# Kernel tuning notes

Hardware: AMD Instinct MI355X
Metric: run time of the kernel (lower is better)

Reference implementation:

```python
import jax, jax.numpy as jnp
import numpy as np

V, D, B, P = 50000, 128, 1024, 50
N, E = B * P, B * P
SCALE = 12.0


def _norm(x):
    return jnp.linalg.norm(x, axis=-1, keepdims=True)


def setup_inputs():
    key = jax.random.key(0)
    ks = jax.random.split(key, 32)
    stdv = 1.0 / np.sqrt(D)

    def u(k, shape):
        return jax.random.uniform(k, shape, minval=-stdv, maxval=stdv, dtype=jnp.float32)

    iid = jax.random.randint(ks[0], (N,), 0, V)
    # edges stay inside each session's node block [g*P, (g+1)*P)
    base = jnp.repeat(jnp.arange(B) * P, P)
    edge_src = base + jax.random.randint(ks[1], (E,), 0, P)
    edge_dst = base + jax.random.randint(ks[2], (E,), 0, P)
    node_gid = jnp.repeat(jnp.arange(B), P)          # session id per node
    last_nodes = jnp.arange(B) * P + (P - 1)          # nodes with data['last']==1
    edge_w = jax.random.uniform(ks[3], (E,), minval=0.1, maxval=1.0)
    edge_t = jax.random.uniform(ks[4], (E,))
    params = dict(
        embedding=u(ks[5], (V, D)),
        W1=u(ks[6], (D, 2 * D)), W2=u(ks[7], (D, 2 * D)),
        gru_wih=u(ks[8], (3 * D, 4 * D)), gru_whh=u(ks[9], (3 * D, D)),
        gru_bih=u(ks[10], (3 * D,)), gru_bhh=u(ks[11], (3 * D,)),
        Wxr=u(ks[12], (D, D)), bxr=u(ks[13], (D,)),
        Wxz=u(ks[14], (D, D)), bxz=u(ks[15], (D,)),
        Wxh=u(ks[16], (D, D)), bxh=u(ks[17], (D,)),
        Whr=u(ks[18], (D, D)), bhr=u(ks[19], (D,)),
        Whz=u(ks[20], (D, D)), bhz=u(ks[21], (D,)),
        Whh=u(ks[22], (D, D)), bhh=u(ks[23], (D,)),
        fc_u=u(ks[24], (D, D)),
        fc_vw=u(ks[25], (D, D)), fc_vb=u(ks[26], (D,)),
        fc_e=u(ks[27], (D,)),
        fc_sr=u(ks[28], (2 * D, D)),
    )
    return dict(iid=iid, edge_src=edge_src, edge_dst=edge_dst, node_gid=node_gid,
                last_nodes=last_nodes, edge_w=edge_w, edge_t=edge_t, **params)


def reference(iid, edge_src, edge_dst, node_gid, last_nodes, edge_w, edge_t,
              embedding, W1, W2, gru_wih, gru_whh, gru_bih, gru_bhh,
              Wxr, bxr, Wxz, bxz, Wxh, bxh, Whr, bhr, Whz, bhz, Whh, bhh,
              fc_u, fc_vw, fc_vb, fc_e, fc_sr):
    segN = lambda d, ids: jax.ops.segment_sum(d, ids, num_segments=N)
    feat = embedding[iid]
    feat = feat / (_norm(feat) + 1e-12)

    # --- GGNNLayer (num_layers=1): weighted-mean over in-edges and reversed graph ---
    ws_in = segN(edge_w, edge_dst)
    ws_out = segN(edge_w, edge_src)
    m_in = segN(feat[edge_src] * edge_w[:, None], edge_dst)
    m_out = segN(feat[edge_dst] * edge_w[:, None], edge_src)
    neigh1 = m_in / jnp.where(ws_in > 0, ws_in, 1.0)[:, None]   # zero-degree -> 0 (DGL default)
    neigh2 = m_out / jnp.where(ws_out > 0, ws_out, 1.0)[:, None]
    hn = jnp.concatenate([neigh1 @ W1, neigh2 @ W2], axis=1)    # [N, 4D]
    gi = hn @ gru_wih.T + gru_bih
    gh = feat @ gru_whh.T + gru_bhh
    ir, iz, inn = jnp.split(gi, 3, axis=1)
    hr, hz, hnn = jnp.split(gh, 3, axis=1)
    r = jax.nn.sigmoid(ir + hr)
    z = jax.nn.sigmoid(iz + hz)
    n = jnp.tanh(inn + r * hnn)
    feat = (1.0 - z) * n + z * feat                              # GRUCell update
    feat = feat / jnp.maximum(_norm(feat), 1e-12)                # F.normalize

    # --- GraphGRUODE: one RK4 step on [0, t_end]; per-eval time-filtered symmetric GCN ---
    x = feat
    no_self = edge_src != edge_dst

    def gcn(h, em, W, b):
        # DGL GraphConv norm='both' on the masked graph + its reverse edges
        deg = segN(em, edge_src) + segN(em, edge_dst)
        nrm = jnp.maximum(deg, 1.0) ** -0.5
        hs = h * nrm[:, None]
        me = em[:, None]
        agg = segN(hs[edge_src] * me, edge_dst) + segN(hs[edge_dst] * me, edge_src)
        return (agg * nrm[:, None]) @ W + b

    def f(tv, h):
        em = ((edge_t <= tv) & no_self).astype(h.dtype)
        xr = gcn(x, em, Wxr, bxr)
        xz = gcn(x, em, Wxz, bxz)
        xh = gcn(x, em, Wxh, bxh)
        r_ = jax.nn.sigmoid(xr + gcn(h, em, Whr, bhr))
        z_ = jax.nn.sigmoid(xz + gcn(h, em, Whz, bhz))
        u_ = jnp.tanh(xh + gcn(r_ * h, em, Whh, bhh))
        dh = (1.0 - z_) * (u_ - h)
        return dh / jnp.maximum(_norm(dh), 1e-12)                # F.normalize

    dt = edge_t.max()
    k1 = f(jnp.float32(0.0), feat)
    k2 = f(dt * 0.5, feat + dt * 0.5 * k1)
    k3 = f(dt * 0.5, feat + dt * 0.5 * k2)
    k4 = f(dt, feat + dt * k3)
    feat = feat + (dt / 6.0) * (k1 + 2.0 * k2 + 2.0 * k3 + k4)
    feat = feat / _norm(feat)                                    # torch code divides with no eps here

    # --- AttnReadout (batch_norm disabled, fc_out is None) ---
    fu = feat @ fc_u
    fv = feat[last_nodes] @ fc_vw + fc_vb                        # [B, D]
    e = jax.nn.sigmoid(fu + fv[node_gid]) @ fc_e                 # [N]
    emax = jax.ops.segment_max(e, node_gid, num_segments=B)
    ee = jnp.exp(e - emax[node_gid])
    alpha = ee / jax.ops.segment_sum(ee, node_gid, num_segments=B)[node_gid]
    sr_g = jax.ops.segment_sum(feat * alpha[:, None], node_gid, num_segments=B)
    sr = jnp.concatenate([feat[last_nodes], sr_g], axis=1) @ fc_sr
    sr = sr / (_norm(sr) + 1e-12)

    target = embedding / (_norm(embedding) + 1e-12)
    logits = sr @ target.T                                       # [B, V]
    return jax.nn.log_softmax(SCALE * logits, axis=-1)
```

## Files before the change

kernel.cpp:

```cpp
#include <hip/hip_runtime.h>
#include <math.h>

constexpr int V_ = 50000, D_ = 128, B_ = 1024, P_ = 50;
constexpr int N_ = 51200, E_ = 51200;
constexpr long long NS_ = (long long)N_ * D_;
constexpr float SCALE_ = 12.0f;
constexpr int NBN_L = (V_ + 127) / 128;
constexpr int NBN_P = 392;

typedef unsigned short u16;
typedef __attribute__((ext_vector_type(8))) unsigned short u16x8;
typedef __attribute__((ext_vector_type(8))) __bf16 bf16x8;
typedef __attribute__((ext_vector_type(4))) float f32x4;

static __device__ __forceinline__ float wsum(float v) {
    #pragma unroll
    for (int o = 32; o; o >>= 1) v += __shfl_xor(v, o, 64);
    return v;
}
static __device__ __forceinline__ float wmax(float v) {
    #pragma unroll
    for (int o = 32; o; o >>= 1) v = fmaxf(v, __shfl_xor(v, o, 64));
    return v;
}
static __device__ __forceinline__ float fsig(float x) { return 1.f / (1.f + __expf(-x)); }
static __device__ __forceinline__ float ftanh(float x) { return 2.f / (1.f + __expf(-2.f * x)) - 1.f; }
static __device__ __forceinline__ u16 f2b(float x) {
    unsigned u = __float_as_uint(x);
    u += 0x7fffu + ((u >> 16) & 1u);
    return (u16)(u >> 16);
}
static __device__ __forceinline__ float b2f(u16 u) {
    return __uint_as_float(((unsigned)u) << 16);
}
static __device__ __forceinline__ float redlr(float v) {
    v += __shfl_xor(v, 1, 64); v += __shfl_xor(v, 2, 64);
    v += __shfl_xor(v, 4, 64); v += __shfl_xor(v, 8, 64);
    return v;
}

__global__ void k_embcv(const float* __restrict__ emb, u16* __restrict__ embb,
                        float* __restrict__ rnv) {
    int row = blockIdx.x * 4 + (threadIdx.x >> 6);
    if (row >= V_) return;
    int l = threadIdx.x & 63;
    const float* p = emb + (long long)row * D_;
    float a = p[l], b = p[l + 64];
    float ss = wsum(a * a + b * b);
    if (l == 0) rnv[row] = 1.f / (sqrtf(ss) + 1e-12f);
    u16* q = embb + (long long)row * D_;
    q[l] = f2b(a); q[l + 64] = f2b(b);
}

__global__ void k_dtmax(const float* __restrict__ et, float* __restrict__ dt) {
    __shared__ float s[1024];
    float m = 0.f;
    for (int i = threadIdx.x; i < E_; i += 1024) m = fmaxf(m, et[i]);
    s[threadIdx.x] = m; __syncthreads();
    for (int o = 512; o; o >>= 1) {
        if (threadIdx.x < o) s[threadIdx.x] = fmaxf(s[threadIdx.x], s[threadIdx.x + o]);
        __syncthreads();
    }
    if (threadIdx.x == 0) *dt = s[0];
}

__global__ void k_feat0(const u16* __restrict__ embb, const float* __restrict__ rnv,
                        const int* __restrict__ iid, u16* __restrict__ featb) {
    int row = blockIdx.x * 4 + (threadIdx.x >> 6);
    int l = threadIdx.x & 63;
    int id = iid[row];
    const u16* p = embb + (long long)id * D_;
    float s = rnv[id];
    u16* qb = featb + (long long)row * D_;
    qb[l] = f2b(b2f(p[l]) * s); qb[l + 64] = f2b(b2f(p[l + 64]) * s);
}

__global__ void k_aggA_g(const int* __restrict__ esrc, const int* __restrict__ edst,
                         const float* __restrict__ ew, const u16* __restrict__ featb,
                         u16* __restrict__ m_in, u16* __restrict__ m_out) {
    __shared__ float sfeat[P_ * D_];
    __shared__ float smin[P_ * D_];
    __shared__ float smout[P_ * D_];
    __shared__ int ses[P_], sed[P_];
    __shared__ float sw[P_], swin[P_], swout[P_];
    int g = blockIdx.x, t = threadIdx.x;
    int n0 = g * P_;
    long long base = (long long)n0 * D_;
    for (int i = t; i < P_ * D_; i += 256) {
        sfeat[i] = b2f(featb[base + i]);
        smin[i] = 0.f; smout[i] = 0.f;
    }
    if (t < P_) {
        int E0 = g * P_ + t;
        ses[t] = esrc[E0] - n0;
        sed[t] = edst[E0] - n0;
        sw[t] = ew[E0];
    }
    __syncthreads();
    int d = t & 127;
    for (int e = 0; e < P_; e++) {
        int ls = ses[e], ld = sed[e];
        float w = sw[e];
        if (t < 128) smin[ld * D_ + d] += sfeat[ls * D_ + d] * w;
        else         smout[ls * D_ + d] += sfeat[ld * D_ + d] * w;
    }
    if (t < P_) {
        float wi = 0.f, wo = 0.f;
        for (int e = 0; e < P_; e++) {
            if (sed[e] == t) wi += sw[e];
            if (ses[e] == t) wo += sw[e];
        }
        swin[t] = (wi > 0.f) ? 1.f / wi : 1.f;
        swout[t] = (wo > 0.f) ? 1.f / wo : 1.f;
    }
    __syncthreads();
    for (int i = t; i < P_ * D_; i += 256) {
        int n = i >> 7;
        m_in[base + i] = f2b(smin[i] * swin[n]);
        m_out[base + i] = f2b(smout[i] * swout[n]);
    }
}

__global__ void k_prec_all(const float* __restrict__ W1, const float* __restrict__ W2,
                           const float* __restrict__ wih, const float* __restrict__ whh,
                           const float* __restrict__ bih, const float* __restrict__ bhh,
                           const float* __restrict__ Wxr, const float* __restrict__ Wxz,
                           const float* __restrict__ Whr, const float* __restrict__ Whz,
                           const float* __restrict__ bxr, const float* __restrict__ bxz,
                           const float* __restrict__ bhr, const float* __restrict__ bhz,
                           const float* __restrict__ Wxh, const float* __restrict__ Whh,
                           const float* __restrict__ bxh, const float* __restrict__ bhh2,
                           const float* __restrict__ fcu,
                           u16* __restrict__ BM1t, u16* __restrict__ BM2t, u16* __restrict__ BM3t,
                           u16* __restrict__ Brz1, u16* __restrict__ Brz2,
                           u16* __restrict__ Bu1, u16* __restrict__ Bu2, u16* __restrict__ Bfc,
                           float* __restrict__ b512, float* __restrict__ brz,
                           float* __restrict__ bu) {
    int blk = blockIdx.x, t = threadIdx.x;
    if (blk < 512) {
        const float* W = (blk < 256) ? W1 : W2;
        int coff = (blk < 256) ? 0 : 256;
        u16* Bt = (blk < 256) ? BM1t : BM2t;
        int idx = (blk & 255) * 256 + t;
        int j = idx >> 7, k = idx & 127;
        float s = 0.f;
        if (j < 384) {
            const float* wr = W + (long long)k * 256;
            const float* ir = wih + (long long)j * 512 + coff;
            for (int c = 0; c < 256; c++) s += wr[c] * ir[c];
        }
        Bt[idx] = f2b(s);
    } else if (blk < 768) {
        int idx = (blk - 512) * 256 + t;
        int j = idx >> 7, k = idx & 127;
        float v = 0.f;
        if (j < 256) v = whh[(long long)j * 128 + k];
        else if (j >= 384) v = whh[(long long)(j - 128) * 128 + k];
        BM3t[idx] = f2b(v);
    } else if (blk < 896) {
        int idx = (blk - 768) * 256 + t;
        int c = idx >> 7, k = idx & 127;
        float v1 = (c < 128) ? Wxr[(long long)k * 128 + c] : Wxz[(long long)k * 128 + (c - 128)];
        float v2 = (c < 128) ? Whr[(long long)k * 128 + c] : Whz[(long long)k * 128 + (c - 128)];
        Brz1[idx] = f2b(v1); Brz2[idx] = f2b(v2);
        if (k == 0) brz[c] = (c < 128) ? bxr[c] + bhr[c] : bxz[c - 128] + bhz[c - 128];
    } else if (blk < 960) {
        int idx = (blk - 896) * 256 + t;
        int c = idx >> 7, k = idx & 127;
        Bu1[idx] = f2b(Wxh[(long long)k * 128 + c]);
        Bu2[idx] = f2b(Whh[(long long)k * 128 + c]);
        if (k == 0) bu[c] = bxh[c] + bhh2[c];
    } else if (blk < 1024) {
        int idx = (blk - 960) * 256 + t;
        int c = idx >> 7, k = idx & 127;
        Bfc[idx] = f2b(fcu[(long long)k * 128 + c]);
    } else {
        int j = (blk - 1024) * 256 + t;
        if (j < 512) {
            float v;
            if (j < 256) v = bih[j] + bhh[j];
            else if (j < 384) v = bih[j];
            else v = bhh[j - 128];
            b512[j] = v;
        }
    }
}

template<int NSEG, int ACT>
__launch_bounds__(256)
__global__ void k_mm(const u16* __restrict__ A1, const u16* __restrict__ A2,
                     const u16* __restrict__ A3,
                     const u16* __restrict__ B1, const u16* __restrict__ B2,
                     const u16* __restrict__ B3,
                     const float* __restrict__ bias,
                     u16* __restrict__ C, int ldc, int nbn) {
    __shared__ u16 As[128 * 40];
    __shared__ u16 Bs[128 * 40];
    const int t = threadIdx.x;
    const int bid = blockIdx.x;
    const int xcd = bid & 7, idx = bid >> 3;
    const int nbm8 = gridDim.x / (8 * nbn);
    const int bm = xcd * nbm8 + idx / nbn;
    const int bn = idx % nbn;
    const int lane = t & 63, wid = t >> 6;
    const int wr = wid >> 1, wc = wid & 1;
    const int lr = lane & 15, lh = lane >> 4;
    f32x4 acc[4][4] = {};
    constexpr int KTOT = NSEG * 128;
    for (int ks = 0; ks < KTOT; ks += 32) {
        const u16* Ap = (NSEG == 1) ? A1 : (ks < 128 ? A1 : (ks < 256 ? A2 : A3));
        const u16* Bp = (NSEG == 1) ? B1 : (ks < 128 ? B1 : (ks < 256 ? B2 : B3));
        int kk = ks & 127;
        #pragma unroll
        for (int i = 0; i < 2; i++) {
            int id2 = i * 256 + t;
            int row = id2 >> 2, kl = (id2 & 3) * 8;
            u16x8 va = *(const u16x8*)&Ap[((long long)bm * 128 + row) * 128 + kk + kl];
            *(u16x8*)&As[row * 40 + kl] = va;
            u16x8 vb = *(const u16x8*)&Bp[((long long)bn * 128 + row) * 128 + kk + kl];
            *(u16x8*)&Bs[row * 40 + kl] = vb;
        }
        __syncthreads();
        bf16x8 af[4], bf[4];
        #pragma unroll
        for (int f = 0; f < 4; f++) {
            u16x8 ar = *(const u16x8*)&As[(wr * 64 + f * 16 + lr) * 40 + lh * 8];
            u16x8 br = *(const u16x8*)&Bs[(wc * 64 + f * 16 + lr) * 40 + lh * 8];
            af[f] = __builtin_bit_cast(bf16x8, ar);
            bf[f] = __builtin_bit_cast(bf16x8, br);
        }
        #pragma unroll
        for (int fr = 0; fr < 4; fr++)
            #pragma unroll
            for (int fc = 0; fc < 4; fc++)
                acc[fr][fc] = __builtin_amdgcn_mfma_f32_16x16x32_bf16(af[fr], bf[fc], acc[fr][fc], 0, 0, 0);
        __syncthreads();
    }
    #pragma unroll
    for (int fc = 0; fc < 4; fc++) {
        int col = bn * 128 + wc * 64 + fc * 16 + lr;
        float bb = bias ? bias[col] : 0.f;
        #pragma unroll
        for (int fr = 0; fr < 4; fr++) {
            int rowl = wr * 64 + fr * 16 + lh * 4;
            long long row0 = (long long)bm * 128 + rowl;
            #pragma unroll
            for (int r = 0; r < 4; r++) {
                float v = acc[fr][fc][r] + bb;
                if (ACT == 1) v = fsig(v);
                else if (ACT == 2) v = ftanh(v);
                C[(row0 + r) * (long long)ldc + col] = f2b(v);
            }
        }
    }
}

__global__ void k_gru2(const u16* __restrict__ gih, u16* __restrict__ featb,
                       u16* __restrict__ hb) {
    int row = blockIdx.x * 4 + (threadIdx.x >> 6);
    int l = threadIdx.x & 63;
    const u16* g = gih + (long long)row * 512;
    u16* fb = featb + (long long)row * 128;
    float nv[2]; float ss = 0.f;
    #pragma unroll
    for (int tq = 0; tq < 2; tq++) {
        int d = l + tq * 64;
        float r = fsig(b2f(g[d]));
        float z = fsig(b2f(g[128 + d]));
        float n = ftanh(b2f(g[256 + d]) + r * b2f(g[384 + d]));
        float fv = b2f(fb[d]);
        nv[tq] = (1.f - z) * n + z * fv;
        ss += nv[tq] * nv[tq];
    }
    ss = wsum(ss);
    float s = 1.f / fmaxf(sqrtf(ss), 1e-12f);
    u16 a = f2b(nv[0] * s), b = f2b(nv[1] * s);
    fb[l] = a; fb[l + 64] = b;
    u16* hh = hb + (long long)row * 128;
    hh[l] = a; hh[l + 64] = b;
}

template<int FIN>
__launch_bounds__(512, 8)
__global__ void k_fstep(const int* __restrict__ esrc, const int* __restrict__ edst,
                        const float* __restrict__ et, const float* __restrict__ dtp,
                        float tfac, int h_is_x, int axmode,
                        u16* __restrict__ featb, u16* __restrict__ hb,
                        u16* __restrict__ AXg, u16* __restrict__ RHG, u16* __restrict__ ZG,
                        float* __restrict__ accg,
                        const u16* __restrict__ Brz1, const u16* __restrict__ Brz2,
                        const float* __restrict__ brz,
                        const u16* __restrict__ Bu1, const u16* __restrict__ Bu2,
                        const float* __restrict__ bu,
                        float accw, float hfac, int first) {
    constexpr int AS = 136;
    __shared__ u16 sAX[64 * AS];
    __shared__ u16 sAH[64 * AS];
    __shared__ float snrm[P_];
    __shared__ int ses[P_], sed[P_], sdeg[P_], soff[P_ + 1], snbr[2 * P_];
    __shared__ float ssqW[4][64];
    const int g = blockIdx.x, t = threadIdx.x;
    const int n0 = g * P_;
    const long long base = (long long)n0 * D_;
    const int wv = t >> 6, lane = t & 63;
    const int lr = lane & 15, lh = lane >> 4;
    const float dt = dtp[0];
    const float tv = tfac * dt;

    for (int i = t; i < 64 * AS; i += 512) { sAX[i] = 0; sAH[i] = 0; }
    if (t < P_) {
        int E0 = g * P_ + t;
        int ss_ = esrc[E0] - n0, dd = edst[E0] - n0;
        bool ml = (ss_ != dd) && (et[E0] <= tv);
        ses[t] = ml ? ss_ : -1;
        sed[t] = ml ? dd : -1;
    }
    __syncthreads();
    if (t < P_) {
        int dg = 0;
        for (int e = 0; e < P_; e++) dg += (ses[e] == t) + (sed[e] == t);
        sdeg[t] = dg;
        snrm[t] = rsqrtf(fmaxf((float)dg, 1.f));
    }
    __syncthreads();
    if (t < 64) {
        int v = (t < P_) ? sdeg[t] : 0;
        int inc = v;
        #pragma unroll
        for (int o = 1; o < 64; o <<= 1) {
            int u = __shfl_up(inc, o, 64);
            if (t >= o) inc += u;
        }
        if (t < P_) soff[t] = inc - v;
        if (t == P_ - 1) soff[P_] = inc;
    }
    __syncthreads();
    if (t < P_) {
        int c = soff[t];
        for (int e = 0; e < P_; e++) {
            if (ses[e] == t) snbr[c++] = sed[e];
            if (sed[e] == t) snbr[c++] = ses[e];
        }
    }
    __syncthreads();

    const int d = t & 127, grp = t >> 7;
    const int nlo = grp * 13, nhi = (grp * 13 + 13 < P_) ? grp * 13 + 13 : P_;
    if (axmode == 2) {
        for (int n = nlo; n < nhi; n++)
            sAX[n * AS + d] = AXg[base + (long long)n * D_ + d];
    } else {
        for (int n = nlo; n < nhi; n++) {
            float a = 0.f;
            for (int j = soff[n]; j < soff[n + 1]; j++) {
                int nb = snbr[j];
                a += b2f(featb[base + (long long)nb * D_ + d]) * snrm[nb];
            }
            u16 v = f2b(a * snrm[n]);
            sAX[n * AS + d] = v;
            if (axmode == 1) AXg[base + (long long)n * D_ + d] = v;
        }
    }
    if (!h_is_x) {
        for (int n = nlo; n < nhi; n++) {
            float a = 0.f;
            for (int j = soff[n]; j < soff[n + 1]; j++) {
                int nb = snbr[j];
                a += b2f(hb[base + (long long)nb * D_ + d]) * snrm[nb];
            }
            sAH[n * AS + d] = f2b(a * snrm[n]);
        }
    }
    __syncthreads();
    {
        const u16* A2 = h_is_x ? sAX : sAH;
        f32x4 acc[4][2] = {};
        for (int ks = 0; ks < 256; ks += 32) {
            const u16* Ap = (ks < 128) ? sAX : A2;
            const u16* Bp = (ks < 128) ? Brz1 : Brz2;
            int kk = ks & 127;
            bf16x8 af[4], bf[2];
            #pragma unroll
            for (int f = 0; f < 4; f++) {
                u16x8 ar = *(const u16x8*)&Ap[(f * 16 + lr) * AS + kk + lh * 8];
                af[f] = __builtin_bit_cast(bf16x8, ar);
            }
            #pragma unroll
            for (int f = 0; f < 2; f++) {
                int col = wv * 32 + f * 16 + lr;
                u16x8 br = *(const u16x8*)&Bp[(long long)col * 128 + kk + lh * 8];
                bf[f] = __builtin_bit_cast(bf16x8, br);
            }
            #pragma unroll
            for (int fr = 0; fr < 4; fr++)
                #pragma unroll
                for (int fc = 0; fc < 2; fc++)
                    acc[fr][fc] = __builtin_amdgcn_mfma_f32_16x16x32_bf16(af[fr], bf[fc], acc[fr][fc], 0, 0, 0);
        }
        #pragma unroll
        for (int fc = 0; fc < 2; fc++) {
            int col = wv * 32 + fc * 16 + lr;
            float bb = brz[col];
            #pragma unroll
            for (int fr = 0; fr < 4; fr++) {
                int row0 = fr * 16 + lh * 4;
                #pragma unroll
                for (int r = 0; r < 4; r++) {
                    int row = row0 + r;
                    if (row < P_) {
                        float v = fsig(acc[fr][fc][r] + bb);
                        long long ix = base + (long long)row * D_;
                        if (col < 128) RHG[ix + col] = f2b(v * b2f(hb[ix + col]));
                        else           ZG[ix + col - 128] = f2b(v);
                    }
                }
            }
        }
    }
    __syncthreads();
    for (int n = nlo; n < nhi; n++) {
        float a = 0.f;
        for (int j = soff[n]; j < soff[n + 1]; j++) {
            int nb = snbr[j];
            a += b2f(RHG[base + (long long)nb * D_ + d]) * snrm[nb];
        }
        sAH[n * AS + d] = f2b(a * snrm[n]);
    }
    __syncthreads();
    const int wr = wv >> 2, wc = wv & 3;
    f32x4 acc[2][2] = {};
    for (int ks = 0; ks < 256; ks += 32) {
        const u16* Ap = (ks < 128) ? sAX : sAH;
        const u16* Bp = (ks < 128) ? Bu1 : Bu2;
        int kk = ks & 127;
        bf16x8 af[2], bf[2];
        #pragma unroll
        for (int f = 0; f < 2; f++) {
            u16x8 ar = *(const u16x8*)&Ap[(wr * 32 + f * 16 + lr) * AS + kk + lh * 8];
            af[f] = __builtin_bit_cast(bf16x8, ar);
        }
        #pragma unroll
        for (int f = 0; f < 2; f++) {
            int col = wc * 32 + f * 16 + lr;
            u16x8 br = *(const u16x8*)&Bp[(long long)col * 128 + kk + lh * 8];
            bf[f] = __builtin_bit_cast(bf16x8, br);
        }
        #pragma unroll
        for (int fr = 0; fr < 2; fr++)
            #pragma unroll
            for (int fc = 0; fc < 2; fc++)
                acc[fr][fc] = __builtin_amdgcn_mfma_f32_16x16x32_bf16(af[fr], bf[fc], acc[fr][fc], 0, 0, 0);
    }
    float pr[2][4] = {};
    #pragma unroll
    for (int fc = 0; fc < 2; fc++) {
        int col = wc * 32 + fc * 16 + lr;
        float bb = bu[col];
        #pragma unroll
        for (int fr = 0; fr < 2; fr++) {
            int row0 = wr * 32 + fr * 16 + lh * 4;
            #pragma unroll
            for (int r = 0; r < 4; r++) {
                int row = row0 + r;
                float v = 0.f;
                if (row < P_) {
                    long long ix = base + (long long)row * D_ + col;
                    float u = ftanh(acc[fr][fc][r] + bb);
                    float z = b2f(ZG[ix]);
                    float hh = b2f(hb[ix]);
                    v = (1.f - z) * (u - hh);
                }
                acc[fr][fc][r] = v;
                pr[fr][r] += v * v;
            }
        }
    }
    #pragma unroll
    for (int fr = 0; fr < 2; fr++)
        #pragma unroll
        for (int r = 0; r < 4; r++) {
            float v = redlr(pr[fr][r]);
            if (lr == 0) ssqW[wc][wr * 32 + fr * 16 + lh * 4 + r] = v;
        }
    __syncthreads();
    if (FIN) {
        float dt6 = dt / 6.f;
        float pr2[2][4] = {};
        #pragma unroll
        for (int fr = 0; fr < 2; fr++) {
            int row0 = wr * 32 + fr * 16 + lh * 4;
            #pragma unroll
            for (int r = 0; r < 4; r++) {
                int row = row0 + r;
                float sc = 0.f;
                if (row < P_) {
                    float ssum = ssqW[0][row] + ssqW[1][row] + ssqW[2][row] + ssqW[3][row];
                    sc = 1.f / fmaxf(sqrtf(ssum), 1e-12f);
                }
                #pragma unroll
                for (int fc = 0; fc < 2; fc++) {
                    int col = wc * 32 + fc * 16 + lr;
                    float fv2 = 0.f;
                    if (row < P_) {
                        long long ix = base + (long long)row * D_ + col;
                        float kv = acc[fr][fc][r] * sc;
                        float an = accg[ix] + accw * kv;
                        fv2 = b2f(featb[ix]) + dt6 * an;
                    }
                    acc[fr][fc][r] = fv2;
                    pr2[fr][r] += fv2 * fv2;
                }
            }
        }
        __syncthreads();
        #pragma unroll
        for (int fr = 0; fr < 2; fr++)
            #pragma unroll
            for (int r = 0; r < 4; r++) {
                float v = redlr(pr2[fr][r]);
                if (lr == 0) ssqW[wc][wr * 32 + fr * 16 + lh * 4 + r] = v;
            }
        __syncthreads();
        #pragma unroll
        for (int fr = 0; fr < 2; fr++) {
            int row0 = wr * 32 + fr * 16 + lh * 4;
            #pragma unroll
            for (int r = 0; r < 4; r++) {
                int row = row0 + r;
                if (row >= P_) continue;
                float ssum = ssqW[0][row] + ssqW[1][row] + ssqW[2][row] + ssqW[3][row];
                float s2 = 1.f / sqrtf(ssum);
                #pragma unroll
                for (int fc = 0; fc < 2; fc++) {
                    int col = wc * 32 + fc * 16 + lr;
                    featb[base + (long long)row * D_ + col] = f2b(acc[fr][fc][r] * s2);
                }
            }
        }
    } else {
        #pragma unroll
        for (int fr = 0; fr < 2; fr++) {
            int row0 = wr * 32 + fr * 16 + lh * 4;
            #pragma unroll
            for (int r = 0; r < 4; r++) {
                int row = row0 + r;
                if (row >= P_) continue;
                float ssum = ssqW[0][row] + ssqW[1][row] + ssqW[2][row] + ssqW[3][row];
                float sc = 1.f / fmaxf(sqrtf(ssum), 1e-12f);
                #pragma unroll
                for (int fc = 0; fc < 2; fc++) {
                    int col = wc * 32 + fc * 16 + lr;
                    long long ix = base + (long long)row * D_ + col;
                    float kv = acc[fr][fc][r] * sc;
                    float an = (first ? 0.f : accg[ix]) + accw * kv;
                    accg[ix] = an;
                    hb[ix] = f2b(b2f(featb[ix]) + hfac * dt * kv);
                }
            }
        }
    }
}

__launch_bounds__(256)
__global__ void k_readout(const u16* __restrict__ featb, const u16* __restrict__ FU,
                          const int* __restrict__ last,
                          const float* __restrict__ fvw, const float* __restrict__ fvbv,
                          const float* __restrict__ fce, const float* __restrict__ fsr,
                          u16* __restrict__ srb) {
    __shared__ float sfl[128], sfv[128], se[64], sal[64], sin2[256], red[2];
    int g = blockIdx.x, t = threadIdx.x;
    int n0 = g * P_;
    long long ln = last[g];
    if (t < 128) sfl[t] = b2f(featb[ln * 128 + t]);
    __syncthreads();
    if (t < 128) {
        float s = fvbv[t];
        for (int k = 0; k < 128; k++) s += sfl[k] * fvw[(long long)k * 128 + t];
        sfv[t] = s;
        sin2[t] = sfl[t];
    }
    __syncthreads();
    int wid = t >> 6, lane = t & 63;
    float fce0 = fce[lane], fce1 = fce[lane + 64];
    for (int p = wid; p < P_; p += 4) {
        const u16* fu = FU + (long long)(n0 + p) * 128;
        float x0 = b2f(fu[lane]) + sfv[lane];
        float x1 = b2f(fu[lane + 64]) + sfv[lane + 64];
        float s = fsig(x0) * fce0 + fsig(x1) * fce1;
        s = wsum(s);
        if (lane == 0) se[p] = s;
    }
    __syncthreads();
    if (t < 64) {
        float v = (t < P_) ? se[t] : -1e30f;
        float m = wmax(v);
        float ex = (t < P_) ? __expf(v - m) : 0.f;
        float ss = wsum(ex);
        if (t < P_) sal[t] = ex / ss;
    }
    __syncthreads();
    if (t < 128) {
        float s = 0.f;
        for (int p = 0; p < P_; p++)
            s += b2f(featb[(long long)(n0 + p) * 128 + t]) * sal[p];
        sin2[128 + t] = s;
    }
    __syncthreads();
    if (t < 128) {
        float s = 0.f;
        for (int k = 0; k < 256; k++) s += sin2[k] * fsr[(long long)k * 128 + t];
        float ss = wsum(s * s);
        if (lane == 0) red[t >> 6] = ss;
        __syncthreads();
        float nrm = sqrtf(red[0] + red[1]);
        srb[(long long)g * 128 + t] = f2b(s / (nrm + 1e-12f));
    } else {
        __syncthreads();
    }
}

template<int PASS>
__launch_bounds__(256)
__global__ void k_logits(const u16* __restrict__ A, const u16* __restrict__ Bt,
                         const float* __restrict__ rnv, float* __restrict__ rowsumP,
                         const float* __restrict__ logz, float* __restrict__ C) {
    __shared__ u16 As[128 * 40];
    __shared__ u16 Bs[128 * 40];
    __shared__ float sredW[2][128];
    const int t = threadIdx.x;
    const int bid = blockIdx.x;
    const int xcd = bid & 7, idx = bid >> 3;
    const int bm = idx & 7, bnl = idx >> 3;
    const int bn = xcd * 49 + bnl;
    if (bn >= NBN_L) return;
    const int lane = t & 63, wid = t >> 6;
    const int wr = wid >> 1, wc = wid & 1;
    const int lr = lane & 15, lh = lane >> 4;
    f32x4 acc[4][4] = {};
    for (int ks = 0; ks < 128; ks += 32) {
        #pragma unroll
        for (int i = 0; i < 2; i++) {
            int id2 = i * 256 + t;
            int row = id2 >> 2, kl = (id2 & 3) * 8;
            u16x8 va = *(const u16x8*)&A[((long long)bm * 128 + row) * 128 + ks + kl];
            *(u16x8*)&As[row * 40 + kl] = va;
            long long gcol = (long long)bn * 128 + row;
            u16x8 vb;
            if (gcol < V_) vb = *(const u16x8*)&Bt[gcol * 128 + ks + kl];
            else vb = u16x8{0, 0, 0, 0, 0, 0, 0, 0};
            *(u16x8*)&Bs[row * 40 + kl] = vb;
        }
        __syncthreads();
        bf16x8 af[4], bf[4];
        #pragma unroll
        for (int f = 0; f < 4; f++) {
            u16x8 ar = *(const u16x8*)&As[(wr * 64 + f * 16 + lr) * 40 + lh * 8];
            u16x8 br = *(const u16x8*)&Bs[(wc * 64 + f * 16 + lr) * 40 + lh * 8];
            af[f] = __builtin_bit_cast(bf16x8, ar);
            bf[f] = __builtin_bit_cast(bf16x8, br);
        }
        #pragma unroll
        for (int fr = 0; fr < 4; fr++)
            #pragma unroll
            for (int fc = 0; fc < 4; fc++)
                acc[fr][fc] = __builtin_amdgcn_mfma_f32_16x16x32_bf16(af[fr], bf[fc], acc[fr][fc], 0, 0, 0);
        __syncthreads();
    }
    if (PASS == 0) {
        float pr[4][4] = {};
        #pragma unroll
        for (int fc = 0; fc < 4; fc++) {
            int col = bn * 128 + wc * 64 + fc * 16 + lr;
            if (col >= V_) continue;
            float cs = rnv[col] * SCALE_;
            #pragma unroll
            for (int fr = 0; fr < 4; fr++)
                #pragma unroll
                for (int r = 0; r < 4; r++)
                    pr[fr][r] += __expf(acc[fr][fc][r] * cs - SCALE_);
        }
        #pragma unroll
        for (int fr = 0; fr < 4; fr++)
            #pragma unroll
            for (int r = 0; r < 4; r++) {
                float v = redlr(pr[fr][r]);
                if (lr == 0) sredW[wc][wr * 64 + fr * 16 + lh * 4 + r] = v;
            }
        __syncthreads();
        if (t < 128) rowsumP[(long long)(bm * 128 + t) * NBN_P + bn] = sredW[0][t] + sredW[1][t];
    } else {
        if (t < 128) sredW[0][t] = logz[bm * 128 + t];
        __syncthreads();
        #pragma unroll
        for (int fc = 0; fc < 4; fc++) {
            int col = bn * 128 + wc * 64 + fc * 16 + lr;
            if (col >= V_) continue;
            float cs = rnv[col] * SCALE_;
            #pragma unroll
            for (int fr = 0; fr < 4; fr++) {
                int rowl = wr * 64 + fr * 16 + lh * 4;
                long long row0 = (long long)bm * 128 + rowl;
                #pragma unroll
                for (int r = 0; r < 4; r++)
                    C[(row0 + r) * (long long)V_ + col] = acc[fr][fc][r] * cs - SCALE_ - sredW[0][rowl + r];
            }
        }
    }
}

__global__ void k_rsum(const float* __restrict__ rowsumP, float* __restrict__ logz) {
    int t = threadIdx.x;
    int row = blockIdx.x * 128 + (t >> 1);
    int half = t & 1;
    const float* p = rowsumP + (long long)row * NBN_P;
    float s = 0.f;
    int j0 = half ? 196 : 0, j1 = half ? NBN_L : 196;
    for (int j = j0; j < j1; j++) s += p[j];
    s += __shfl_xor(s, 1);
    if (!half) logz[row] = logf(s);
}

extern "C" void kernel_launch(void* const* d_in, const int* in_sizes, int n_in,
                              void* d_out, int out_size, void* d_ws, size_t ws_size,
                              hipStream_t stream) {
    const int* iid   = (const int*)d_in[0];
    const int* esrc  = (const int*)d_in[1];
    const int* edst  = (const int*)d_in[2];
    const int* last  = (const int*)d_in[4];
    const float* ew  = (const float*)d_in[5];
    const float* et  = (const float*)d_in[6];
    const float* emb = (const float*)d_in[7];
    const float* W1  = (const float*)d_in[8];
    const float* W2  = (const float*)d_in[9];
    const float* wih = (const float*)d_in[10];
    const float* whh = (const float*)d_in[11];
    const float* bih = (const float*)d_in[12];
    const float* bhh = (const float*)d_in[13];
    const float* Wxr = (const float*)d_in[14]; const float* bxr = (const float*)d_in[15];
    const float* Wxz = (const float*)d_in[16]; const float* bxz = (const float*)d_in[17];
    const float* Wxh = (const float*)d_in[18]; const float* bxh = (const float*)d_in[19];
    const float* Whr = (const float*)d_in[20]; const float* bhr = (const float*)d_in[21];
    const float* Whz = (const float*)d_in[22]; const float* bhz = (const float*)d_in[23];
    const float* Whh = (const float*)d_in[24]; const float* bhh2 = (const float*)d_in[25];
    const float* fcu = (const float*)d_in[26];
    const float* fvw = (const float*)d_in[27]; const float* fvbv = (const float*)d_in[28];
    const float* fce = (const float*)d_in[29];
    const float* fsr = (const float*)d_in[30];
    float* out = (float*)d_out;

    char* w = (char*)d_ws;
    auto alloc = [&](size_t bytes) { char* p = w; w += (bytes + 255) & ~(size_t)255; return p; };
    float* ACC   = (float*)alloc(NS_ * 4);
    u16* FEATb   = (u16*)alloc(NS_ * 2);
    u16* Hb      = (u16*)alloc(NS_ * 2);
    u16* MINb    = (u16*)alloc(NS_ * 2);
    u16* MOUTb   = (u16*)alloc(NS_ * 2);
    u16* GIHb    = (u16*)alloc(NS_ * 8);
    u16* AXb     = GIHb;
    u16* RHG     = GIHb + NS_;
    u16* ZG      = GIHb + 2 * NS_;
    u16* FUb     = MINb;
    u16* embb    = (u16*)alloc((long long)V_ * 128 * 2);
    u16* srb     = (u16*)alloc(B_ * 128 * 2);
    u16* BM1t    = (u16*)alloc(512 * 128 * 2);
    u16* BM2t    = (u16*)alloc(512 * 128 * 2);
    u16* BM3t    = (u16*)alloc(512 * 128 * 2);
    u16* Brz1    = (u16*)alloc(256 * 128 * 2);
    u16* Brz2    = (u16*)alloc(256 * 128 * 2);
    u16* Bu1     = (u16*)alloc(128 * 128 * 2);
    u16* Bu2     = (u16*)alloc(128 * 128 * 2);
    u16* Bfc     = (u16*)alloc(128 * 128 * 2);
    float* b512  = (float*)alloc(512 * 4);
    float* brz   = (float*)alloc(256 * 4);
    float* bu    = (float*)alloc(128 * 4);
    float* dtp   = (float*)alloc(64 * 4);
    float* rnv   = (float*)alloc((long long)V_ * 4);
    float* rowsumP = (float*)alloc((long long)B_ * NBN_P * 4);
    float* logz  = (float*)alloc(B_ * 4);

    k_embcv<<<(V_ + 3) / 4, 256, 0, stream>>>(emb, embb, rnv);
    k_dtmax<<<1, 1024, 0, stream>>>(et, dtp);
    k_feat0<<<N_ / 4, 256, 0, stream>>>(embb, rnv, iid, FEATb);

    k_aggA_g<<<B_, 256, 0, stream>>>(esrc, edst, ew, FEATb, MINb, MOUTb);
    k_prec_all<<<1026, 256, 0, stream>>>(W1, W2, wih, whh, bih, bhh,
                                         Wxr, Wxz, Whr, Whz, bxr, bxz, bhr, bhz,
                                         Wxh, Whh, bxh, bhh2, fcu,
                                         BM1t, BM2t, BM3t, Brz1, Brz2, Bu1, Bu2, Bfc,
                                         b512, brz, bu);
    k_mm<3, 0><<<1600, 256, 0, stream>>>(MINb, MOUTb, FEATb, BM1t, BM2t, BM3t, b512, GIHb, 512, 4);
    k_gru2<<<N_ / 4, 256, 0, stream>>>(GIHb, FEATb, Hb);

    k_fstep<0><<<B_, 512, 0, stream>>>(esrc, edst, et, dtp, 0.0f, 1, 0, FEATb, Hb, AXb, RHG, ZG,
                                       ACC, Brz1, Brz2, brz, Bu1, Bu2, bu, 1.f, 0.5f, 1);
    k_fstep<0><<<B_, 512, 0, stream>>>(esrc, edst, et, dtp, 0.5f, 0, 1, FEATb, Hb, AXb, RHG, ZG,
                                       ACC, Brz1, Brz2, brz, Bu1, Bu2, bu, 2.f, 0.5f, 0);
    k_fstep<0><<<B_, 512, 0, stream>>>(esrc, edst, et, dtp, 0.5f, 0, 2, FEATb, Hb, AXb, RHG, ZG,
                                       ACC, Brz1, Brz2, brz, Bu1, Bu2, bu, 2.f, 1.0f, 0);
    k_fstep<1><<<B_, 512, 0, stream>>>(esrc, edst, et, dtp, 1.0f, 0, 0, FEATb, Hb, AXb, RHG, ZG,
                                       ACC, Brz1, Brz2, brz, Bu1, Bu2, bu, 1.f, 0.0f, 0);

    k_mm<1, 0><<<400, 256, 0, stream>>>(FEATb, nullptr, nullptr, Bfc, nullptr, nullptr,
                                        nullptr, FUb, 128, 1);
    k_readout<<<B_, 256, 0, stream>>>(FEATb, FUb, last, fvw, fvbv, fce, fsr, srb);

    k_logits<0><<<3136, 256, 0, stream>>>(srb, embb, rnv, rowsumP, nullptr, nullptr);
    k_rsum<<<8, 256, 0, stream>>>(rowsumP, logz);
    k_logits<1><<<3136, 256, 0, stream>>>(srb, embb, rnv, nullptr, logz, out);
}
```

Measured before the change: 680.3 us.

## Fuse four RK4 stage kernels into one persistent per-session kernel

Replaces the four separate k_fstep launches with a single k_rk4 kernel that loops over the four RK4 stages inside each session block. It keeps the AX aggregation in shared memory across stages 1 and 2, so the global AX buffer round-trip and the repeated mask and adjacency rebuild for stage 2 go away. It also reads feat directly as h in stage 0 instead of copying it into Hb in k_gru2. This saves launch gaps and some global traffic, at the cost of a longer kernel with more barriers and possibly more register pressure.

```diff
diff --git a/kernel.cpp b/kernel.cpp
--- a/kernel.cpp
+++ b/kernel.cpp
@@ -255,8 +255,7 @@
     }
 }
 
-__global__ void k_gru2(const u16* __restrict__ gih, u16* __restrict__ featb,
-                       u16* __restrict__ hb) {
+__global__ void k_gru2(const u16* __restrict__ gih, u16* __restrict__ featb) {
     int row = blockIdx.x * 4 + (threadIdx.x >> 6);
     int l = threadIdx.x & 63;
     const u16* g = gih + (long long)row * 512;
@@ -274,25 +273,19 @@
     }
     ss = wsum(ss);
     float s = 1.f / fmaxf(sqrtf(ss), 1e-12f);
-    u16 a = f2b(nv[0] * s), b = f2b(nv[1] * s);
-    fb[l] = a; fb[l + 64] = b;
-    u16* hh = hb + (long long)row * 128;
-    hh[l] = a; hh[l + 64] = b;
-}
-
-template<int FIN>
+    fb[l] = f2b(nv[0] * s); fb[l + 64] = f2b(nv[1] * s);
+}
+
 __launch_bounds__(512, 8)
-__global__ void k_fstep(const int* __restrict__ esrc, const int* __restrict__ edst,
-                        const float* __restrict__ et, const float* __restrict__ dtp,
-                        float tfac, int h_is_x, int axmode,
-                        u16* __restrict__ featb, u16* __restrict__ hb,
-                        u16* __restrict__ AXg, u16* __restrict__ RHG, u16* __restrict__ ZG,
-                        float* __restrict__ accg,
-                        const u16* __restrict__ Brz1, const u16* __restrict__ Brz2,
-                        const float* __restrict__ brz,
-                        const u16* __restrict__ Bu1, const u16* __restrict__ Bu2,
-                        const float* __restrict__ bu,
-                        float accw, float hfac, int first) {
+__global__ void k_rk4(const int* __restrict__ esrc, const int* __restrict__ edst,
+                      const float* __restrict__ et, const float* __restrict__ dtp,
+                      u16* __restrict__ featb, u16* __restrict__ hb,
+                      u16* __restrict__ RHG, u16* __restrict__ ZG,
+                      float* __restrict__ accg,
+                      const u16* __restrict__ Brz1, const u16* __restrict__ Brz2,
+                      const float* __restrict__ brz,
+                      const u16* __restrict__ Bu1, const u16* __restrict__ Bu2,
+                      const float* __restrict__ bu) {
     constexpr int AS = 136;
     __shared__ u16 sAX[64 * AS];
     __shared__ u16 sAH[64 * AS];
@@ -305,259 +298,271 @@
     const int wv = t >> 6, lane = t & 63;
     const int lr = lane & 15, lh = lane >> 4;
     const float dt = dtp[0];
-    const float tv = tfac * dt;
 
     for (int i = t; i < 64 * AS; i += 512) { sAX[i] = 0; sAH[i] = 0; }
-    if (t < P_) {
-        int E0 = g * P_ + t;
-        int ss_ = esrc[E0] - n0, dd = edst[E0] - n0;
-        bool ml = (ss_ != dd) && (et[E0] <= tv);
-        ses[t] = ml ? ss_ : -1;
-        sed[t] = ml ? dd : -1;
-    }
-    __syncthreads();
-    if (t < P_) {
-        int dg = 0;
-        for (int e = 0; e < P_; e++) dg += (ses[e] == t) + (sed[e] == t);
-        sdeg[t] = dg;
-        snrm[t] = rsqrtf(fmaxf((float)dg, 1.f));
-    }
-    __syncthreads();
-    if (t < 64) {
-        int v = (t < P_) ? sdeg[t] : 0;
-        int inc = v;
-        #pragma unroll
-        for (int o = 1; o < 64; o <<= 1) {
-            int u = __shfl_up(inc, o, 64);
-            if (t >= o) inc += u;
-        }
-        if (t < P_) soff[t] = inc - v;
-        if (t == P_ - 1) soff[P_] = inc;
-    }
-    __syncthreads();
-    if (t < P_) {
-        int c = soff[t];
-        for (int e = 0; e < P_; e++) {
-            if (ses[e] == t) snbr[c++] = sed[e];
-            if (sed[e] == t) snbr[c++] = ses[e];
-        }
-    }
     __syncthreads();
 
     const int d = t & 127, grp = t >> 7;
     const int nlo = grp * 13, nhi = (grp * 13 + 13 < P_) ? grp * 13 + 13 : P_;
-    if (axmode == 2) {
-        for (int n = nlo; n < nhi; n++)
-            sAX[n * AS + d] = AXg[base + (long long)n * D_ + d];
-    } else {
+
+    for (int s = 0; s < 4; s++) {
+        const float tfac = (s == 0) ? 0.f : ((s == 3) ? 1.f : 0.5f);
+        const float accw = (s == 1 || s == 2) ? 2.f : 1.f;
+        const float hfac = (s <= 1) ? 0.5f : ((s == 2) ? 1.f : 0.f);
+        const int h_is_x = (s == 0);
+        const int skip_mask = (s == 2);
+        const u16* hcur = h_is_x ? featb : hb;
+        const float tv = tfac * dt;
+
+        if (!skip_mask) {
+            if (t < P_) {
+                int E0 = g * P_ + t;
+                int ss_ = esrc[E0] - n0, dd = edst[E0] - n0;
+                bool ml = (ss_ != dd) && (et[E0] <= tv);
+                ses[t] = ml ? ss_ : -1;
+                sed[t] = ml ? dd : -1;
+            }
+            __syncthreads();
+            if (t < P_) {
+                int dg = 0;
+                for (int e = 0; e < P_; e++) dg += (ses[e] == t) + (sed[e] == t);
+                sdeg[t] = dg;
+                snrm[t] = rsqrtf(fmaxf((float)dg, 1.f));
+            }
+            __syncthreads();
+            if (t < 64) {
+                int v = (t < P_) ? sdeg[t] : 0;
+                int inc = v;
+                #pragma unroll
+                for (int o = 1; o < 64; o <<= 1) {
+                    int u = __shfl_up(inc, o, 64);
+                    if (t >= o) inc += u;
+                }
+                if (t < P_) soff[t] = inc - v;
+                if (t == P_ - 1) soff[P_] = inc;
+            }
+            __syncthreads();
+            if (t < P_) {
+                int c = soff[t];
+                for (int e = 0; e < P_; e++) {
+                    if (ses[e] == t) snbr[c++] = sed[e];
+                    if (sed[e] == t) snbr[c++] = ses[e];
+                }
+            }
+            __syncthreads();
+        }
+
+        if (!skip_mask) {
+            for (int n = nlo; n < nhi; n++) {
+                float a = 0.f;
+                for (int j = soff[n]; j < soff[n + 1]; j++) {
+                    int nb = snbr[j];
+                    a += b2f(featb[base + (long long)nb * D_ + d]) * snrm[nb];
+                }
+                sAX[n * AS + d] = f2b(a * snrm[n]);
+            }
+        }
+        if (!h_is_x) {
+            for (int n = nlo; n < nhi; n++) {
+                float a = 0.f;
+                for (int j = soff[n]; j < soff[n + 1]; j++) {
+                    int nb = snbr[j];
+                    a += b2f(hcur[base + (long long)nb * D_ + d]) * snrm[nb];
+                }
+                sAH[n * AS + d] = f2b(a * snrm[n]);
+            }
+        }
+        __syncthreads();
+        {
+            const u16* A2 = h_is_x ? sAX : sAH;
+            f32x4 acc[4][2] = {};
+            for (int ks = 0; ks < 256; ks += 32) {
+                const u16* Ap = (ks < 128) ? sAX : A2;
+                const u16* Bp = (ks < 128) ? Brz1 : Brz2;
+                int kk = ks & 127;
+                bf16x8 af[4], bf[2];
+                #pragma unroll
+                for (int f = 0; f < 4; f++) {
+                    u16x8 ar = *(const u16x8*)&Ap[(f * 16 + lr) * AS + kk + lh * 8];
+                    af[f] = __builtin_bit_cast(bf16x8, ar);
+                }
+                #pragma unroll
+                for (int f = 0; f < 2; f++) {
+                    int col = wv * 32 + f * 16 + lr;
+                    u16x8 br = *(const u16x8*)&Bp[(long long)col * 128 + kk + lh * 8];
+                    bf[f] = __builtin_bit_cast(bf16x8, br);
+                }
+                #pragma unroll
+                for (int fr = 0; fr < 4; fr++)
+                    #pragma unroll
+                    for (int fc = 0; fc < 2; fc++)
+                        acc[fr][fc] = __builtin_amdgcn_mfma_f32_16x16x32_bf16(af[fr], bf[fc], acc[fr][fc], 0, 0, 0);
+            }
+            #pragma unroll
+            for (int fc = 0; fc < 2; fc++) {
+                int col = wv * 32 + fc * 16 + lr;
+                float bb = brz[col];
+                #pragma unroll
+                for (int fr = 0; fr < 4; fr++) {
+                    int row0 = fr * 16 + lh * 4;
+                    #pragma unroll
+                    for (int r = 0; r < 4; r++) {
+                        int row = row0 + r;
+                        if (row < P_) {
+                            float v = fsig(acc[fr][fc][r] + bb);
+                            long long ix = base + (long long)row * D_;
+                            if (col < 128) RHG[ix + col] = f2b(v * b2f(hcur[ix + col]));
+                            else           ZG[ix + col - 128] = f2b(v);
+                        }
+                    }
+                }
+            }
+        }
+        __syncthreads();
         for (int n = nlo; n < nhi; n++) {
             float a = 0.f;
             for (int j = soff[n]; j < soff[n + 1]; j++) {
                 int nb = snbr[j];
-                a += b2f(featb[base + (long long)nb * D_ + d]) * snrm[nb];
-            }
-            u16 v = f2b(a * snrm[n]);
-            sAX[n * AS + d] = v;
-            if (axmode == 1) AXg[base + (long long)n * D_ + d] = v;
-        }
-    }
-    if (!h_is_x) {
-        for (int n = nlo; n < nhi; n++) {
-            float a = 0.f;
-            for (int j = soff[n]; j < soff[n + 1]; j++) {
-                int nb = snbr[j];
-                a += b2f(hb[base + (long long)nb * D_ + d]) * snrm[nb];
+                a += b2f(RHG[base + (long long)nb * D_ + d]) * snrm[nb];
             }
             sAH[n * AS + d] = f2b(a * snrm[n]);
         }
-    }
-    __syncthreads();
-    {
-        const u16* A2 = h_is_x ? sAX : sAH;
-        f32x4 acc[4][2] = {};
-        for (int ks = 0; ks < 256; ks += 32) {
-            const u16* Ap = (ks < 128) ? sAX : A2;
-            const u16* Bp = (ks < 128) ? Brz1 : Brz2;
-            int kk = ks & 127;
-            bf16x8 af[4], bf[2];
+        __syncthreads();
+        {
+            const int wr = wv >> 2, wc = wv & 3;
+            f32x4 acc[2][2] = {};
+            for (int ks = 0; ks < 256; ks += 32) {
+                const u16* Ap = (ks < 128) ? sAX : sAH;
+                const u16* Bp = (ks < 128) ? Bu1 : Bu2;
+                int kk = ks & 127;
+                bf16x8 af[2], bf[2];
+                #pragma unroll
+                for (int f = 0; f < 2; f++) {
+                    u16x8 ar = *(const u16x8*)&Ap[(wr * 32 + f * 16 + lr) * AS + kk + lh * 8];
+                    af[f] = __builtin_bit_cast(bf16x8, ar);
+                }
+                #pragma unroll
+                for (int f = 0; f < 2; f++) {
+                    int col = wc * 32 + f * 16 + lr;
+                    u16x8 br = *(const u16x8*)&Bp[(long long)col * 128 + kk + lh * 8];
+                    bf[f] = __builtin_bit_cast(bf16x8, br);
+                }
+                #pragma unroll
+                for (int fr = 0; fr < 2; fr++)
+                    #pragma unroll
+                    for (int fc = 0; fc < 2; fc++)
+                        acc[fr][fc] = __builtin_amdgcn_mfma_f32_16x16x32_bf16(af[fr], bf[fc], acc[fr][fc], 0, 0, 0);
+            }
+            float pr[2][4] = {};
             #pragma unroll
-            for (int f = 0; f < 4; f++) {
-                u16x8 ar = *(const u16x8*)&Ap[(f * 16 + lr) * AS + kk + lh * 8];
-                af[f] = __builtin_bit_cast(bf16x8, ar);
+            for (int fc = 0; fc < 2; fc++) {
+                int col = wc * 32 + fc * 16 + lr;
+                float bb = bu[col];
+                #pragma unroll
+                for (int fr = 0; fr < 2; fr++) {
+                    int row0 = wr * 32 + fr * 16 + lh * 4;
+                    #pragma unroll
+                    for (int r = 0; r < 4; r++) {
+                        int row = row0 + r;
+                        float v = 0.f;
+                        if (row < P_) {
+                            long long ix = base + (long long)row * D_ + col;
+                            float u = ftanh(acc[fr][fc][r] + bb);
+                            float z = b2f(ZG[ix]);
+                            float hh = b2f(hcur[ix]);
+                            v = (1.f - z) * (u - hh);
+                        }
+                        acc[fr][fc][r] = v;
+                        pr[fr][r] += v * v;
+                    }
+                }
             }
             #pragma unroll
-            for (int f = 0; f < 2; f++) {
-                int col = wv * 32 + f * 16 + lr;
-                u16x8 br = *(const u16x8*)&Bp[(long long)col * 128 + kk + lh * 8];
-                bf[f] = __builtin_bit_cast(bf16x8, br);
-            }
-            #pragma unroll
-            for (int fr = 0; fr < 4; fr++)
-                #pragma unroll
-                for (int fc = 0; fc < 2; fc++)
-                    acc[fr][fc] = __builtin_amdgcn_mfma_f32_16x16x32_bf16(af[fr], bf[fc], acc[fr][fc], 0, 0, 0);
-        }
-        #pragma unroll
-        for (int fc = 0; fc < 2; fc++) {
-            int col = wv * 32 + fc * 16 + lr;
-            float bb = brz[col];
-            #pragma unroll
-            for (int fr = 0; fr < 4; fr++) {
-                int row0 = fr * 16 + lh * 4;
+            for (int fr = 0; fr < 2; fr++)
                 #pragma unroll
                 for (int r = 0; r < 4; r++) {
-                    int row = row0 + r;
-                    if (row < P_) {
-                        float v = fsig(acc[fr][fc][r] + bb);
-                        long long ix = base + (long long)row * D_;
-                        if (col < 128) RHG[ix + col] = f2b(v * b2f(hb[ix + col]));
-                        else           ZG[ix + col - 128] = f2b(v);
+                    float v = redlr(pr[fr][r]);
+                    if (lr == 0) ssqW[wc][wr * 32 + fr * 16 + lh * 4 + r] = v;
+                }
+            __syncthreads();
+            if (s == 3) {
+                float dt6 = dt / 6.f;
+                float pr2[2][4] = {};
+                #pragma unroll
+                for (int fr = 0; fr < 2; fr++) {
+                    int row0 = wr * 32 + fr * 16 + lh * 4;
+                    #pragma unroll
+                    for (int r = 0; r < 4; r++) {
+                        int row = row0 + r;
+                        float sc = 0.f;
+                        if (row < P_) {
+                            float ssum = ssqW[0][row] + ssqW[1][row] + ssqW[2][row] + ssqW[3][row];
+                            sc = 1.f / fmaxf(sqrtf(ssum), 1e-12f);
+                        }
+                        #pragma unroll
+                        for (int fc = 0; fc < 2; fc++) {
+                            int col = wc * 32 + fc * 16 + lr;
+                            float fv2 = 0.f;
+                            if (row < P_) {
+                                long long ix = base + (long long)row * D_ + col;
+                                float kv = acc[fr][fc][r] * sc;
+                                float an = accg[ix] + accw * kv;
+                                fv2 = b2f(featb[ix]) + dt6 * an;
+                            }
+                            acc[fr][fc][r] = fv2;
+                            pr2[fr][r] += fv2 * fv2;
+                        }
                     }
                 }
-            }
-        }
-    }
-    __syncthreads();
-    for (int n = nlo; n < nhi; n++) {
-        float a = 0.f;
-        for (int j = soff[n]; j < soff[n + 1]; j++) {
-            int nb = snbr[j];
-            a += b2f(RHG[base + (long long)nb * D_ + d]) * snrm[nb];
-        }
-        sAH[n * AS + d] = f2b(a * snrm[n]);
-    }
-    __syncthreads();
-    const int wr = wv >> 2, wc = wv & 3;
-    f32x4 acc[2][2] = {};
-    for (int ks = 0; ks < 256; ks += 32) {
-        const u16* Ap = (ks < 128) ? sAX : sAH;
-        const u16* Bp = (ks < 128) ? Bu1 : Bu2;
-        int kk = ks & 127;
-        bf16x8 af[2], bf[2];
-        #pragma unroll
-        for (int f = 0; f < 2; f++) {
-            u16x8 ar = *(const u16x8*)&Ap[(wr * 32 + f * 16 + lr) * AS + kk + lh * 8];
-            af[f] = __builtin_bit_cast(bf16x8, ar);
-        }
-        #pragma unroll
-        for (int f = 0; f < 2; f++) {
-            int col = wc * 32 + f * 16 + lr;
-            u16x8 br = *(const u16x8*)&Bp[(long long)col * 128 + kk + lh * 8];
-            bf[f] = __builtin_bit_cast(bf16x8, br);
-        }
-        #pragma unroll
-        for (int fr = 0; fr < 2; fr++)
-            #pragma unroll
-            for (int fc = 0; fc < 2; fc++)
-                acc[fr][fc] = __builtin_amdgcn_mfma_f32_16x16x32_bf16(af[fr], bf[fc], acc[fr][fc], 0, 0, 0);
-    }
-    float pr[2][4] = {};
-    #pragma unroll
-    for (int fc = 0; fc < 2; fc++) {
-        int col = wc * 32 + fc * 16 + lr;
-        float bb = bu[col];
-        #pragma unroll
-        for (int fr = 0; fr < 2; fr++) {
-            int row0 = wr * 32 + fr * 16 + lh * 4;
-            #pragma unroll
-            for (int r = 0; r < 4; r++) {
-                int row = row0 + r;
-                float v = 0.f;
-                if (row < P_) {
-                    long long ix = base + (long long)row * D_ + col;
-                    float u = ftanh(acc[fr][fc][r] + bb);
-                    float z = b2f(ZG[ix]);
-                    float hh = b2f(hb[ix]);
-                    v = (1.f - z) * (u - hh);
-                }
-                acc[fr][fc][r] = v;
-                pr[fr][r] += v * v;
-            }
-        }
-    }
-    #pragma unroll
-    for (int fr = 0; fr < 2; fr++)
-        #pragma unroll
-        for (int r = 0; r < 4; r++) {
-            float v = redlr(pr[fr][r]);
-            if (lr == 0) ssqW[wc][wr * 32 + fr * 16 + lh * 4 + r] = v;
-        }
-    __syncthreads();
-    if (FIN) {
-        float dt6 = dt / 6.f;
-        float pr2[2][4] = {};
-        #pragma unroll
-        for (int fr = 0; fr < 2; fr++) {
-            int row0 = wr * 32 + fr * 16 + lh * 4;
-            #pragma unroll
-            for (int r = 0; r < 4; r++) {
-                int row = row0 + r;
-                float sc = 0.f;
-                if (row < P_) {
-                    float ssum = ssqW[0][row] + ssqW[1][row] + ssqW[2][row] + ssqW[3][row];
-                    sc = 1.f / fmaxf(sqrtf(ssum), 1e-12f);
-                }
-                #pragma unroll
-                for (int fc = 0; fc < 2; fc++) {
-                    int col = wc * 32 + fc * 16 + lr;
-                    float fv2 = 0.f;
-                    if (row < P_) {
-                        long long ix = base + (long long)row * D_ + col;
-                        float kv = acc[fr][fc][r] * sc;
-                        float an = accg[ix] + accw * kv;
-                        fv2 = b2f(featb[ix]) + dt6 * an;
+                __syncthreads();
+                #pragma unroll
+                for (int fr = 0; fr < 2; fr++)
+                    #pragma unroll
+                    for (int r = 0; r < 4; r++) {
+                        float v = redlr(pr2[fr][r]);
+                        if (lr == 0) ssqW[wc][wr * 32 + fr * 16 + lh * 4 + r] = v;
                     }
-                    acc[fr][fc][r] = fv2;
-                    pr2[fr][r] += fv2 * fv2;
-                }
-            }
-        }
-        __syncthreads();
-        #pragma unroll
-        for (int fr = 0; fr < 2; fr++)
-            #pragma unroll
-            for (int r = 0; r < 4; r++) {
-                float v = redlr(pr2[fr][r]);
-                if (lr == 0) ssqW[wc][wr * 32 + fr * 16 + lh * 4 + r] = v;
-            }
-        __syncthreads();
-        #pragma unroll
-        for (int fr = 0; fr < 2; fr++) {
-            int row0 = wr * 32 + fr * 16 + lh * 4;
-            #pragma unroll
-            for (int r = 0; r < 4; r++) {
-                int row = row0 + r;
-                if (row >= P_) continue;
-                float ssum = ssqW[0][row] + ssqW[1][row] + ssqW[2][row] + ssqW[3][row];
-                float s2 = 1.f / sqrtf(ssum);
-                #pragma unroll
-                for (int fc = 0; fc < 2; fc++) {
-                    int col = wc * 32 + fc * 16 + lr;
-                    featb[base + (long long)row * D_ + col] = f2b(acc[fr][fc][r] * s2);
-                }
-            }
-        }
-    } else {
-        #pragma unroll
-        for (int fr = 0; fr < 2; fr++) {
-            int row0 = wr * 32 + fr * 16 + lh * 4;
-            #pragma unroll
-            for (int r = 0; r < 4; r++) {
-                int row = row0 + r;
-                if (row >= P_) continue;
-                float ssum = ssqW[0][row] + ssqW[1][row] + ssqW[2][row] + ssqW[3][row];
-                float sc = 1.f / fmaxf(sqrtf(ssum), 1e-12f);
-                #pragma unroll
-                for (int fc = 0; fc < 2; fc++) {
-                    int col = wc * 32 + fc * 16 + lr;
-                    long long ix = base + (long long)row * D_ + col;
-                    float kv = acc[fr][fc][r] * sc;
-                    float an = (first ? 0.f : accg[ix]) + accw * kv;
-                    accg[ix] = an;
-                    hb[ix] = f2b(b2f(featb[ix]) + hfac * dt * kv);
-                }
-            }
-        }
+                __syncthreads();
+                #pragma unroll
+                for (int fr = 0; fr < 2; fr++) {
+                    int row0 = wr * 32 + fr * 16 + lh * 4;
+                    #pragma unroll
+                    for (int r = 0; r < 4; r++) {
+                        int row = row0 + r;
+                        if (row >= P_) continue;
+                        float ssum = ssqW[0][row] + ssqW[1][row] + ssqW[2][row] + ssqW[3][row];
+                        float s2 = 1.f / sqrtf(ssum);
+                        #pragma unroll
+                        for (int fc = 0; fc < 2; fc++) {
+                            int col = wc * 32 + fc * 16 + lr;
+                            featb[base + (long long)row * D_ + col] = f2b(acc[fr][fc][r] * s2);
+                        }
+                    }
+                }
+            } else {
+                #pragma unroll
+                for (int fr = 0; fr < 2; fr++) {
+                    int row0 = wr * 32 + fr * 16 + lh * 4;
+                    #pragma unroll
+                    for (int r = 0; r < 4; r++) {
+                        int row = row0 + r;
+                        if (row >= P_) continue;
+                        float ssum = ssqW[0][row] + ssqW[1][row] + ssqW[2][row] + ssqW[3][row];
+                        float sc = 1.f / fmaxf(sqrtf(ssum), 1e-12f);
+                        #pragma unroll
+                        for (int fc = 0; fc < 2; fc++) {
+                            int col = wc * 32 + fc * 16 + lr;
+                            long long ix = base + (long long)row * D_ + col;
+                            float kv = acc[fr][fc][r] * sc;
+                            float an = ((s == 0) ? 0.f : accg[ix]) + accw * kv;
+                            accg[ix] = an;
+                            hb[ix] = f2b(b2f(featb[ix]) + hfac * dt * kv);
+                        }
+                    }
+                }
+            }
+        }
+        __syncthreads();
     }
 }
 
@@ -756,7 +761,6 @@
     u16* MINb    = (u16*)alloc(NS_ * 2);
     u16* MOUTb   = (u16*)alloc(NS_ * 2);
     u16* GIHb    = (u16*)alloc(NS_ * 8);
-    u16* AXb     = GIHb;
     u16* RHG     = GIHb + NS_;
     u16* ZG      = GIHb + 2 * NS_;
     u16* FUb     = MINb;
@@ -789,16 +793,10 @@
                                          BM1t, BM2t, BM3t, Brz1, Brz2, Bu1, Bu2, Bfc,
                                          b512, brz, bu);
     k_mm<3, 0><<<1600, 256, 0, stream>>>(MINb, MOUTb, FEATb, BM1t, BM2t, BM3t, b512, GIHb, 512, 4);
-    k_gru2<<<N_ / 4, 256, 0, stream>>>(GIHb, FEATb, Hb);
-
-    k_fstep<0><<<B_, 512, 0, stream>>>(esrc, edst, et, dtp, 0.0f, 1, 0, FEATb, Hb, AXb, RHG, ZG,
-                                       ACC, Brz1, Brz2, brz, Bu1, Bu2, bu, 1.f, 0.5f, 1);
-    k_fstep<0><<<B_, 512, 0, stream>>>(esrc, edst, et, dtp, 0.5f, 0, 1, FEATb, Hb, AXb, RHG, ZG,
-                                       ACC, Brz1, Brz2, brz, Bu1, Bu2, bu, 2.f, 0.5f, 0);
-    k_fstep<0><<<B_, 512, 0, stream>>>(esrc, edst, et, dtp, 0.5f, 0, 2, FEATb, Hb, AXb, RHG, ZG,
-                                       ACC, Brz1, Brz2, brz, Bu1, Bu2, bu, 2.f, 1.0f, 0);
-    k_fstep<1><<<B_, 512, 0, stream>>>(esrc, edst, et, dtp, 1.0f, 0, 0, FEATb, Hb, AXb, RHG, ZG,
-                                       ACC, Brz1, Brz2, brz, Bu1, Bu2, bu, 1.f, 0.0f, 0);
+    k_gru2<<<N_ / 4, 256, 0, stream>>>(GIHb, FEATb);
+
+    k_rk4<<<B_, 512, 0, stream>>>(esrc, edst, et, dtp, FEATb, Hb, RHG, ZG, ACC,
+                                  Brz1, Brz2, brz, Bu1, Bu2, bu);
 
     k_mm<1, 0><<<400, 256, 0, stream>>>(FEATb, nullptr, nullptr, Bfc, nullptr, nullptr,
                                         nullptr, FUb, 128, 1);
```

After: 1.419 ms. +108.5%, slower.
